# Kernel optimization log

Hardware: AMD Instinct MI355X
Metric: run time of the kernel (lower is better)

Reference implementation:

```python
import jax, jax.numpy as jnp
import numpy as np

N_GENES = 20000
N_TECH = 2
N_EXP = 4
BATCH = 1024


def setup_inputs() -> dict:
    key = jax.random.key(0)
    k_x, k_w1, k_w2, k_wg = jax.random.split(key, 4)
    R = N_GENES * N_TECH  # number of independent tiny MLPs
    return {
        "x": jax.random.normal(k_x, (BATCH, N_TECH, N_GENES), dtype=jnp.float32),
        "weights1": jax.random.normal(k_w1, (R, N_EXP), dtype=jnp.float32),
        "bias1": jnp.zeros((R, N_EXP), dtype=jnp.float32),
        "weights2": jax.random.normal(k_w2, (R, N_EXP), dtype=jnp.float32),
        "bias2": jnp.zeros((R,), dtype=jnp.float32),
        "weights_g": jax.random.normal(k_wg, (N_GENES, N_TECH), dtype=jnp.float32),
        "bias_g": jnp.zeros((N_GENES,), dtype=jnp.float32),
    }


def reference(x, weights1, bias1, weights2, bias2, weights_g, bias_g):
    B = x.shape[0]
    R = N_GENES * N_TECH
    # --- ParallelBellowsLayers ---
    # x.reshape([-1, 2G]).T -> [R, B]; row r holds (tech=r//G, gene=r%G)
    xr = x.reshape(B, R).T  # [R, B]
    # expand: per-row outer product [R,B,1]@[R,1,E] + bias -> [R,B,E]
    h = jax.nn.relu(xr[:, :, None] * weights1[:, None, :] + bias1[:, None, :])
    # shrink: [R,B,E] @ [R,E] -> [R,B], + per-row bias
    s = jax.nn.relu(jnp.einsum('rbe,re->rb', h, weights2) + bias2[:, None])
    s = s.T.reshape(B, N_TECH, N_GENES)  # [B, T, G]
    # --- ParallelGeneLayers ---
    # per-gene weighted combine across tech: einsum('btg,gt->bg') + bias
    out = jax.nn.relu(jnp.einsum('btg,gt->bg', s, weights_g) + bias_g)
    return out  # [B, G]
```

## Files before the change

### kernel.cpp

```cpp
#include <hip/hip_runtime.h>

#define NG 20000
#define NB 1024

typedef float v4f __attribute__((ext_vector_type(4)));

constexpr int THREADS = 256;
constexpr int GENES_PER_BLOCK = 512;
constexpr int NGB = 40;
constexpr int BB  = 32;
constexpr int NBB = NB / BB;
constexpr int GB_PER_XCD = NGB / 8;

__global__ __launch_bounds__(THREADS, 4)
void cgm_kernel(const float* __restrict__ x,
                const float* __restrict__ w1,
                const float* __restrict__ b1,
                const float* __restrict__ w2,
                const float* __restrict__ b2,
                const float* __restrict__ wg,
                const float* __restrict__ bg,
                float* __restrict__ out)
{
    const int bid = (int)blockIdx.x;
    const int xcd = bid & 7;
    const int j   = bid >> 3;
    const int gb  = xcd * GB_PER_XCD + (j / NBB);
    const int bb  = j % NBB;

    const int lane = (int)threadIdx.x & 63;
    const int wv   = (int)threadIdx.x >> 6;
    const int t    = lane >> 5;
    const int gl   = wv * 32 + (lane & 31);
    const int gbase = gb * GENES_PER_BLOCK + gl * 4;
    if (gbase >= NG) return;

    v4f W1[4], B1[4], W2[4];
    float B2v[4];
    const size_t r0 = (size_t)t * NG + (size_t)gbase;
    #pragma unroll
    for (int g = 0; g < 4; ++g) {
        W1[g]  = *(const v4f*)(w1 + (r0 + g) * 4);
        B1[g]  = *(const v4f*)(b1 + (r0 + g) * 4);
        W2[g]  = *(const v4f*)(w2 + (r0 + g) * 4);
        B2v[g] = b2[r0 + g];
    }
    const v4f wgA = *(const v4f*)(wg + (size_t)gbase * 2);
    const v4f wgB = *(const v4f*)(wg + (size_t)gbase * 2 + 4);
    const v4f bgv = *(const v4f*)(bg + gbase);

    const float* xbase = x + (size_t)t * NG + (size_t)gbase;
    float*       obase = out + (size_t)gbase;

    const int b_lo = bb * BB;
    #pragma unroll 4
    for (int bi = 0; bi < BB; ++bi) {
        const size_t b = (size_t)(b_lo + bi);
        const v4f xv = __builtin_nontemporal_load((const v4f*)(xbase + b * (2 * NG)));

        float s[4];
        #pragma unroll
        for (int g = 0; g < 4; ++g) {
            const float v = xv[g];
            float h, acc = 0.f;
            h = fmaxf(fmaf(v, W1[g].x, B1[g].x), 0.f); acc = fmaf(h, W2[g].x, acc);
            h = fmaxf(fmaf(v, W1[g].y, B1[g].y), 0.f); acc = fmaf(h, W2[g].y, acc);
            h = fmaxf(fmaf(v, W1[g].z, B1[g].z), 0.f); acc = fmaf(h, W2[g].z, acc);
            h = fmaxf(fmaf(v, W1[g].w, B1[g].w), 0.f); acc = fmaf(h, W2[g].w, acc);
            s[g] = fmaxf(acc + B2v[g], 0.f);
        }

        float so[4];
        #pragma unroll
        for (int g = 0; g < 4; ++g) so[g] = __shfl_xor(s[g], 32, 64);

        if (t == 0) {
            v4f o;
            o.x = fmaxf(fmaf(s[0], wgA.x, fmaf(so[0], wgA.y, bgv.x)), 0.f);
            o.y = fmaxf(fmaf(s[1], wgA.z, fmaf(so[1], wgA.w, bgv.y)), 0.f);
            o.z = fmaxf(fmaf(s[2], wgB.x, fmaf(so[2], wgB.y, bgv.z)), 0.f);
            o.w = fmaxf(fmaf(s[3], wgB.z, fmaf(so[3], wgB.w, bgv.w)), 0.f);
            __builtin_nontemporal_store(o, (v4f*)(obase + b * NG));
        }
    }
}

extern "C" void kernel_launch(void* const* d_in, const int* in_sizes, int n_in,
                              void* d_out, int out_size, void* d_ws, size_t ws_size,
                              hipStream_t stream) {
    const float* x  = (const float*)d_in[0];
    const float* w1 = (const float*)d_in[1];
    const float* b1 = (const float*)d_in[2];
    const float* w2 = (const float*)d_in[3];
    const float* b2 = (const float*)d_in[4];
    const float* wg = (const float*)d_in[5];
    const float* bg = (const float*)d_in[6];
    float* out = (float*)d_out;

    dim3 grid(NGB * NBB);
    cgm_kernel<<<grid, THREADS, 0, stream>>>(x, w1, b1, w2, b2, wg, bg, out);
}
```

Before: 54.62 us.

## Process both tech rows per thread and remap grid over batch per XCD

Each thread now handles both tech rows for its 4 genes, loading two x vectors and combining them locally. This removes the cross-half-wave shuffle and the idle half of lanes during the store. The block-to-XCD mapping now splits the batch dimension across XCDs instead of gene blocks, and the batch chunk shrinks to 16. The cost is about twice the weight registers per thread, hence launch bounds drop to 3 waves per SIMD.

```diff
diff --git a/kernel.cpp b/kernel.cpp
--- a/kernel.cpp
+++ b/kernel.cpp
@@ -6,13 +6,14 @@
 typedef float v4f __attribute__((ext_vector_type(4)));
 
 constexpr int THREADS = 256;
-constexpr int GENES_PER_BLOCK = 512;
-constexpr int NGB = 40;
-constexpr int BB  = 32;
+constexpr int GPT = 4;
+constexpr int GPB = THREADS * GPT;
+constexpr int NGB = (NG + GPB - 1) / GPB;
+constexpr int BB  = 16;
 constexpr int NBB = NB / BB;
-constexpr int GB_PER_XCD = NGB / 8;
+constexpr int BB_PER_XCD = NBB / 8;
 
-__global__ __launch_bounds__(THREADS, 4)
+__global__ __launch_bounds__(THREADS, 3)
 void cgm_kernel(const float* __restrict__ x,
                 const float* __restrict__ w1,
                 const float* __restrict__ b1,
@@ -25,63 +26,62 @@
     const int bid = (int)blockIdx.x;
     const int xcd = bid & 7;
     const int j   = bid >> 3;
-    const int gb  = xcd * GB_PER_XCD + (j / NBB);
-    const int bb  = j % NBB;
+    const int gb  = j % NGB;
+    const int bb  = xcd * BB_PER_XCD + j / NGB;
 
-    const int lane = (int)threadIdx.x & 63;
-    const int wv   = (int)threadIdx.x >> 6;
-    const int t    = lane >> 5;
-    const int gl   = wv * 32 + (lane & 31);
-    const int gbase = gb * GENES_PER_BLOCK + gl * 4;
+    const int gbase = gb * GPB + (int)threadIdx.x * GPT;
     if (gbase >= NG) return;
 
-    v4f W1[4], B1[4], W2[4];
-    float B2v[4];
-    const size_t r0 = (size_t)t * NG + (size_t)gbase;
+    v4f W1[2][4], B1[2][4], W2[2][4];
+    float B2v[2][4];
     #pragma unroll
-    for (int g = 0; g < 4; ++g) {
-        W1[g]  = *(const v4f*)(w1 + (r0 + g) * 4);
-        B1[g]  = *(const v4f*)(b1 + (r0 + g) * 4);
-        W2[g]  = *(const v4f*)(w2 + (r0 + g) * 4);
-        B2v[g] = b2[r0 + g];
+    for (int t = 0; t < 2; ++t) {
+        const size_t r0 = (size_t)t * NG + (size_t)gbase;
+        #pragma unroll
+        for (int g = 0; g < 4; ++g) {
+            W1[t][g]  = *(const v4f*)(w1 + (r0 + g) * 4);
+            B1[t][g]  = *(const v4f*)(b1 + (r0 + g) * 4);
+            W2[t][g]  = *(const v4f*)(w2 + (r0 + g) * 4);
+            B2v[t][g] = b2[r0 + g];
+        }
     }
     const v4f wgA = *(const v4f*)(wg + (size_t)gbase * 2);
     const v4f wgB = *(const v4f*)(wg + (size_t)gbase * 2 + 4);
     const v4f bgv = *(const v4f*)(bg + gbase);
 
-    const float* xbase = x + (size_t)t * NG + (size_t)gbase;
-    float*       obase = out + (size_t)gbase;
+    const float* xb0 = x + (size_t)gbase;
+    float*       ob  = out + (size_t)gbase;
 
     const int b_lo = bb * BB;
     #pragma unroll 4
     for (int bi = 0; bi < BB; ++bi) {
         const size_t b = (size_t)(b_lo + bi);
-        const v4f xv = __builtin_nontemporal_load((const v4f*)(xbase + b * (2 * NG)));
+        const float* xr = xb0 + b * (2 * NG);
+        const v4f x0 = __builtin_nontemporal_load((const v4f*)xr);
+        const v4f x1 = __builtin_nontemporal_load((const v4f*)(xr + NG));
 
-        float s[4];
+        float s[2][4];
         #pragma unroll
-        for (int g = 0; g < 4; ++g) {
-            const float v = xv[g];
-            float h, acc = 0.f;
-            h = fmaxf(fmaf(v, W1[g].x, B1[g].x), 0.f); acc = fmaf(h, W2[g].x, acc);
-            h = fmaxf(fmaf(v, W1[g].y, B1[g].y), 0.f); acc = fmaf(h, W2[g].y, acc);
-            h = fmaxf(fmaf(v, W1[g].z, B1[g].z), 0.f); acc = fmaf(h, W2[g].z, acc);
-            h = fmaxf(fmaf(v, W1[g].w, B1[g].w), 0.f); acc = fmaf(h, W2[g].w, acc);
-            s[g] = fmaxf(acc + B2v[g], 0.f);
+        for (int t = 0; t < 2; ++t) {
+            const v4f xv = (t == 0) ? x0 : x1;
+            #pragma unroll
+            for (int g = 0; g < 4; ++g) {
+                const float v = xv[g];
+                float h, acc = 0.f;
+                h = fmaxf(fmaf(v, W1[t][g].x, B1[t][g].x), 0.f); acc = fmaf(h, W2[t][g].x, acc);
+                h = fmaxf(fmaf(v, W1[t][g].y, B1[t][g].y), 0.f); acc = fmaf(h, W2[t][g].y, acc);
+                h = fmaxf(fmaf(v, W1[t][g].z, B1[t][g].z), 0.f); acc = fmaf(h, W2[t][g].z, acc);
+                h = fmaxf(fmaf(v, W1[t][g].w, B1[t][g].w), 0.f); acc = fmaf(h, W2[t][g].w, acc);
+                s[t][g] = fmaxf(acc + B2v[t][g], 0.f);
+            }
         }
 
-        float so[4];
-        #pragma unroll
-        for (int g = 0; g < 4; ++g) so[g] = __shfl_xor(s[g], 32, 64);
-
-        if (t == 0) {
-            v4f o;
-            o.x = fmaxf(fmaf(s[0], wgA.x, fmaf(so[0], wgA.y, bgv.x)), 0.f);
-            o.y = fmaxf(fmaf(s[1], wgA.z, fmaf(so[1], wgA.w, bgv.y)), 0.f);
-            o.z = fmaxf(fmaf(s[2], wgB.x, fmaf(so[2], wgB.y, bgv.z)), 0.f);
-            o.w = fmaxf(fmaf(s[3], wgB.z, fmaf(so[3], wgB.w, bgv.w)), 0.f);
-            __builtin_nontemporal_store(o, (v4f*)(obase + b * NG));
-        }
+        v4f o;
+        o.x = fmaxf(fmaf(s[0][0], wgA.x, fmaf(s[1][0], wgA.y, bgv.x)), 0.f);
+        o.y = fmaxf(fmaf(s[0][1], wgA.z, fmaf(s[1][1], wgA.w, bgv.y)), 0.f);
+        o.z = fmaxf(fmaf(s[0][2], wgB.x, fmaf(s[1][2], wgB.y, bgv.z)), 0.f);
+        o.w = fmaxf(fmaf(s[0][3], wgB.z, fmaf(s[1][3], wgB.w, bgv.w)), 0.f);
+        __builtin_nontemporal_store(o, (v4f*)(ob + b * NG));
     }
 }
 
```

Result: slower. 58.00 us (+6.2%).
